# Kernel optimization log

Measured on AMD Instinct MI355X. Metric: run time of the kernel, lower is better.

Reference implementation:

```python
import jax, jax.numpy as jnp
import numpy as np

N_NODES = 100000


def gcn_conv(x, edge_index, W, b):
    # PyG GCNConv: add self-loops, symmetric normalization, then scatter-add.
    n = x.shape[0]
    loops = jnp.arange(n, dtype=edge_index.dtype)
    src = jnp.concatenate([edge_index[0], loops])
    dst = jnp.concatenate([edge_index[1], loops])
    h = x @ W  # [N, F_out] -- transform before propagate (small GEMM)
    ones = jnp.ones(src.shape[0], dtype=x.dtype)
    deg = jax.ops.segment_sum(ones, dst, num_segments=n)  # in-degree incl. self-loop
    dinv = jnp.where(deg > 0, jax.lax.rsqrt(deg), 0.0)
    norm = dinv[src] * dinv[dst]  # [E+N]
    msg = h[src] * norm[:, None]  # gather + scale, [E+N, F_out]
    out = jax.ops.segment_sum(msg, dst, num_segments=n)  # scatter-add
    return out + b


def setup_inputs() -> dict:
    key = jax.random.key(0)
    k1, k2, k3, k4 = jax.random.split(key, 4)
    d = 128
    x = jax.random.normal(k1, (N_NODES, d), dtype=jnp.float32)
    edge_index = jax.random.randint(k2, (2, 1600000), 0, N_NODES, dtype=jnp.int64)
    scale = 1.0 / np.sqrt(d)
    W1 = jax.random.normal(k3, (d, d), dtype=jnp.float32) * scale
    b1 = jnp.zeros((d,), dtype=jnp.float32)
    W2 = jax.random.normal(k4, (d, d), dtype=jnp.float32) * scale
    b2 = jnp.zeros((d,), dtype=jnp.float32)
    return {"x": x, "edge_index": edge_index, "W1": W1, "b1": b1, "W2": W2, "b2": b2}


def reference(x, edge_index, W1, b1, W2, b2):
    # Layer 1: GCNConv -> relu -> dropout(eval: identity)
    h = jax.nn.relu(gcn_conv(x, edge_index, W1, b1))
    # Layer 2
    h = jax.nn.relu(gcn_conv(h, edge_index, W2, b2))
    return h
```

## Files before the change

kernel.cpp:

```cpp
#include <hip/hip_runtime.h>


#define NFEAT 128
#define BSH 7
#define MAXNB 1024
#define BCAP 4096
#define BPITCH 136
#define EPITCH 132

typedef __attribute__((ext_vector_type(8))) short s8v;
typedef __attribute__((ext_vector_type(4))) float f4v;
typedef __attribute__((ext_vector_type(2))) float f2v;
typedef __attribute__((ext_vector_type(4))) uint u4v;

__device__ inline ushort f2bf(float f) {
    union { float f; uint u; } x; x.f = f;
    uint u = x.u;
    return (ushort)((u + 0x7fffu + ((u >> 16) & 1u)) >> 16);
}
__device__ inline f2v unpk(uint u) {
    union { uint u; float f; } lo, hi;
    lo.u = u << 16;
    hi.u = u & 0xffff0000u;
    return (f2v){lo.f, hi.f};
}
__device__ inline void upadd2(uint4 v, f2v* a) {
    a[0] += unpk(v.x);
    a[1] += unpk(v.y);
    a[2] += unpk(v.z);
    a[3] += unpk(v.w);
}

__global__ __launch_bounds__(256) void k_bscatter(const int* __restrict__ src,
                                                  const int* __restrict__ dst,
                                                  int* __restrict__ gcnt,
                                                  uint* __restrict__ ebuf,
                                                  int E, int NB, int CH) {
    __shared__ int h[MAXNB];
    int t = threadIdx.x;
    for (int i = t; i < NB; i += 256) h[i] = 0;
    __syncthreads();
    int e0 = blockIdx.x * CH;
    int e1 = min(e0 + CH, E);
    for (int e = e0 + t; e < e1; e += 256) atomicAdd(&h[dst[e] >> BSH], 1);
    __syncthreads();
    for (int i = t; i < NB; i += 256) {
        int c = h[i];
        h[i] = c ? (i * BCAP + atomicAdd(&gcnt[i], c)) : 0;
    }
    __syncthreads();
    for (int e = e0 + t; e < e1; e += 256) {
        int d = dst[e];
        int b = d >> BSH;
        int p = atomicAdd(&h[b], 1);
        if (p < (b + 1) * BCAP)
            ebuf[p] = ((uint)src[e] << BSH) | (uint)(d & ((1 << BSH) - 1));
    }
}

__global__ __launch_bounds__(256) void k_fill2(const uint* __restrict__ ebuf,
                                               const int* __restrict__ gcnt,
                                               int* __restrict__ row_ptr,
                                               float* __restrict__ dinv,
                                               int* __restrict__ col,
                                               int N, int E, int NB) {
    __shared__ int cnt[128];
    __shared__ int pre[128];
    __shared__ int sred[256];
    __shared__ int colL[BCAP];
    int b = blockIdx.x;
    int t = threadIdx.x;
    int part = 0;
    for (int j = t; j < b; j += 256) part += gcnt[j];
    sred[t] = part;
    __syncthreads();
    for (int off = 128; off >= 1; off >>= 1) {
        if (t < off) sred[t] += sred[t + off];
        __syncthreads();
    }
    int gb = sred[0];
    int m = min(gcnt[b], BCAP);
    if (t < 128) cnt[t] = 0;
    __syncthreads();
    const uint* eb = ebuf + (size_t)b * BCAP;
    for (int i = t; i < m; i += 256) atomicAdd(&cnt[eb[i] & 127], 1);
    __syncthreads();
    if (t < 128) pre[t] = cnt[t];
    __syncthreads();
    for (int off = 1; off < 128; off <<= 1) {
        int add = (t >= off && t < 128) ? pre[t - off] : 0;
        __syncthreads();
        if (t < 128) pre[t] += add;
        __syncthreads();
    }
    if (t < 128) {
        pre[t] -= cnt[t];
        int node = (b << BSH) + t;
        if (node < N) {
            row_ptr[node] = gb + pre[t];
            dinv[node] = rsqrtf((float)(cnt[t] + 1));
        }
    }
    __syncthreads();
    for (int i = t; i < m; i += 256) {
        uint p = eb[i];
        int pos = atomicAdd(&pre[p & 127], 1);
        colL[pos] = (int)(p >> BSH);
    }
    __syncthreads();
    for (int i = t; i < m; i += 256) col[gb + i] = colL[i];
    if (b == NB - 1 && t == 0) row_ptr[N] = E;
}

template <bool ABF16>
__global__ __launch_bounds__(256) void k_gemm3(const void* __restrict__ Ap,
                                               const float* __restrict__ W,
                                               const float* __restrict__ dinv,
                                               ushort* __restrict__ hs, int M) {
    __shared__ ushort Bs[128 * BPITCH];
    int t = threadIdx.x;

#pragma unroll
    for (int i = 0; i < 16; i++) {
        int idx = t + i * 256;
        int k4 = idx >> 7;
        int n = idx & 127;
        ushort o[4];
#pragma unroll
        for (int j = 0; j < 4; j++) o[j] = f2bf(W[(k4 * 4 + j) * NFEAT + n]);
        uint2 pk;
        __builtin_memcpy(&pk, o, 8);
        *(uint2*)&Bs[n * BPITCH + k4 * 4] = pk;
    }
    __syncthreads();

    int w = t >> 6, l = t & 63;
    int q = l >> 4, ln = l & 15;
    int wid = blockIdx.x * 4 + w;
    int row0 = wid * 32;
    bool alive = row0 < M;
    if (!alive) row0 = (M - 32) & ~31;

    s8v afr[2][4];
#pragma unroll
    for (int mt = 0; mt < 2; mt++) {
        int row = row0 + mt * 16 + ln;
        if (row >= M) row = M - 1;
        if (ABF16) {
            const ushort* A = (const ushort*)Ap + (size_t)row * NFEAT + q * 8;
#pragma unroll
            for (int ks = 0; ks < 4; ks++)
                afr[mt][ks] = *(const s8v*)(A + ks * 32);
        } else {
            const float* A = (const float*)Ap + (size_t)row * NFEAT + q * 8;
#pragma unroll
            for (int ks = 0; ks < 4; ks++) {
                float4 f0 = *(const float4*)(A + ks * 32);
                float4 f1 = *(const float4*)(A + ks * 32 + 4);
                ushort o[8] = {f2bf(f0.x), f2bf(f0.y), f2bf(f0.z), f2bf(f0.w),
                               f2bf(f1.x), f2bf(f1.y), f2bf(f1.z), f2bf(f1.w)};
                __builtin_memcpy(&afr[mt][ks], o, 16);
            }
        }
    }

    f4v acc[2][8];
#pragma unroll
    for (int mt = 0; mt < 2; mt++)
#pragma unroll
        for (int nt = 0; nt < 8; nt++) acc[mt][nt] = (f4v){0.f, 0.f, 0.f, 0.f};
#pragma unroll
    for (int nt = 0; nt < 8; nt++) {
        const ushort* Bp = Bs + (nt * 16 + ln) * BPITCH + q * 8;
#pragma unroll
        for (int ks = 0; ks < 4; ks++) {
            s8v bfr = *(const s8v*)(Bp + ks * 32);
            acc[0][nt] = __builtin_amdgcn_mfma_f32_16x16x32_bf16(afr[0][ks], bfr, acc[0][nt], 0, 0, 0);
            acc[1][nt] = __builtin_amdgcn_mfma_f32_16x16x32_bf16(afr[1][ks], bfr, acc[1][nt], 0, 0, 0);
        }
    }
    __syncthreads();

    ushort* ow = Bs + w * 32 * EPITCH;
#pragma unroll
    for (int mt = 0; mt < 2; mt++) {
#pragma unroll
        for (int r = 0; r < 4; r++) {
            int lrow = mt * 16 + q * 4 + r;
            float d = dinv[row0 + lrow];
#pragma unroll
            for (int nt = 0; nt < 8; nt++)
                ow[lrow * EPITCH + nt * 16 + ln] = f2bf(acc[mt][nt][r] * d);
        }
    }
    __builtin_amdgcn_s_waitcnt(0);
#pragma unroll
    for (int i = 0; i < 8; i++) {
        int idx = l + i * 64;
        int r = idx >> 4, c = idx & 15;
        const ushort* p = ow + r * EPITCH + c * 8;
        uint2 lo = *(const uint2*)p;
        uint2 hi = *(const uint2*)(p + 4);
        uint4 v = make_uint4(lo.x, lo.y, hi.x, hi.y);
        if (alive) *(uint4*)(hs + (size_t)(row0 + r) * NFEAT + c * 8) = v;
    }
}

template <bool OUT_BF16>
__global__ __launch_bounds__(256) void k_aggregate(const uint4* __restrict__ hs4,
                                                   const int* __restrict__ row_ptr,
                                                   const int* __restrict__ col,
                                                   const float* __restrict__ dinv,
                                                   const float* __restrict__ bias,
                                                   void* __restrict__ outp, int N) {
    int node = blockIdx.x * 16 + (threadIdx.x >> 4);
    if (node >= N) return;
    int sub = threadIdx.x & 15;

    uint4 vself = hs4[(size_t)node * 16 + sub];
    int s = row_ptr[node], e = row_ptr[node + 1];
    int nb = (e - s) >> 2;

    f2v a[4];
#pragma unroll
    for (int j = 0; j < 4; j++) a[j] = (f2v){0.f, 0.f};

    int k = s;
    if (nb > 0) {
        int c0 = col[k], c1 = col[k + 1], c2 = col[k + 2], c3 = col[k + 3];
        uint4 v0 = hs4[(size_t)c0 * 16 + sub];
        uint4 v1 = hs4[(size_t)c1 * 16 + sub];
        uint4 v2 = hs4[(size_t)c2 * 16 + sub];
        uint4 v3 = hs4[(size_t)c3 * 16 + sub];
        int d0 = col[k + 4], d1 = col[k + 5], d2 = col[k + 6], d3 = col[k + 7];
        k += 8;
        upadd2(vself, a);
        for (int it = 1; it < nb; ++it, k += 4) {
            uint4 w0 = hs4[(size_t)d0 * 16 + sub];
            uint4 w1 = hs4[(size_t)d1 * 16 + sub];
            uint4 w2 = hs4[(size_t)d2 * 16 + sub];
            uint4 w3 = hs4[(size_t)d3 * 16 + sub];
            int t0 = col[k], t1 = col[k + 1], t2 = col[k + 2], t3 = col[k + 3];
            upadd2(v0, a); upadd2(v1, a); upadd2(v2, a); upadd2(v3, a);
            v0 = w0; v1 = w1; v2 = w2; v3 = w3;
            d0 = t0; d1 = t1; d2 = t2; d3 = t3;
        }
        upadd2(v0, a); upadd2(v1, a); upadd2(v2, a); upadd2(v3, a);
        k = s + nb * 4;
    } else {
        upadd2(vself, a);
    }
    for (; k < e; ++k) upadd2(hs4[(size_t)col[k] * 16 + sub], a);

    float di = dinv[node];
    const float4* b4 = (const float4*)bias;
    float4 b0 = b4[sub * 2], b1 = b4[sub * 2 + 1];
    float r[8];
    r[0] = fmaxf(fmaf(di, a[0].x, b0.x), 0.f);
    r[1] = fmaxf(fmaf(di, a[0].y, b0.y), 0.f);
    r[2] = fmaxf(fmaf(di, a[1].x, b0.z), 0.f);
    r[3] = fmaxf(fmaf(di, a[1].y, b0.w), 0.f);
    r[4] = fmaxf(fmaf(di, a[2].x, b1.x), 0.f);
    r[5] = fmaxf(fmaf(di, a[2].y, b1.y), 0.f);
    r[6] = fmaxf(fmaf(di, a[3].x, b1.z), 0.f);
    r[7] = fmaxf(fmaf(di, a[3].y, b1.w), 0.f);
    if (OUT_BF16) {
        ushort o[8];
#pragma unroll
        for (int j = 0; j < 8; j++) o[j] = f2bf(r[j]);
        u4v pk;
        __builtin_memcpy(&pk, o, 16);
        __builtin_nontemporal_store(pk, (u4v*)outp + (size_t)node * 16 + sub);
    } else {
        float* orow = (float*)outp + (size_t)node * NFEAT + sub * 8;
        f4v r0 = {r[0], r[1], r[2], r[3]};
        f4v r1 = {r[4], r[5], r[6], r[7]};
        __builtin_nontemporal_store(r0, (f4v*)orow);
        __builtin_nontemporal_store(r1, (f4v*)(orow + 4));
    }
}

extern "C" void kernel_launch(void* const* d_in, const int* in_sizes, int n_in,
                              void* d_out, int out_size, void* d_ws, size_t ws_size,
                              hipStream_t stream) {
    const float* x = (const float*)d_in[0];
    const int* ei = (const int*)d_in[1];
    const float* W1 = (const float*)d_in[2];
    const float* b1 = (const float*)d_in[3];
    const float* W2 = (const float*)d_in[4];
    const float* b2 = (const float*)d_in[5];
    float* out = (float*)d_out;

    const int N = in_sizes[0] / NFEAT;
    const int E = in_sizes[1] / 2;
    const int* src = ei;
    const int* dst = ei + E;
    const int NB = (N + (1 << BSH) - 1) >> BSH;

    char* w = (char*)d_ws;
    size_t off = 0;
    auto alloc = [&](size_t bytes) -> void* {
        void* p = w + off;
        off = (off + bytes + 511) & ~(size_t)511;
        return p;
    };
    ushort* hs = (ushort*)alloc((size_t)N * NFEAT * 2);
    ushort* y1 = (ushort*)alloc((size_t)N * NFEAT * 2);
    int* row_ptr = (int*)alloc((size_t)(N + 1) * 4);
    float* dinv = (float*)alloc((size_t)N * 4);
    int* col = (int*)alloc((size_t)E * 4);
    uint* ebuf = (uint*)alloc((size_t)NB * BCAP * 4);
    int* gcnt = (int*)alloc((size_t)MAXNB * 4);
    (void)ws_size; (void)n_in; (void)out_size;

    const int CH = 2048;
    const int chBlk = (E + CH - 1) / CH;

    hipMemsetAsync(gcnt, 0, (size_t)MAXNB * 4, stream);
    k_bscatter<<<chBlk, 256, 0, stream>>>(src, dst, gcnt, ebuf, E, NB, CH);
    k_fill2<<<NB, 256, 0, stream>>>(ebuf, gcnt, row_ptr, dinv, col, N, E, NB);

    const int gemmBlk = (N + 127) / 128;
    const int aggBlk = (N + 15) / 16;

    k_gemm3<false><<<gemmBlk, 256, 0, stream>>>(x, W1, dinv, hs, N);
    k_aggregate<true><<<aggBlk, 256, 0, stream>>>((const uint4*)hs, row_ptr, col, dinv, b1, y1, N);
    k_gemm3<true><<<gemmBlk, 256, 0, stream>>>(y1, W2, dinv, hs, N);
    k_aggregate<false><<<aggBlk, 256, 0, stream>>>((const uint4*)hs, row_ptr, col, dinv, b2, out, N);
}
```

Before: 317.1 us.

## Overlap first GEMM with edge bucketing by moving dinv scaling into aggregation

The source-side dinv scaling moves out of the GEMM epilogue and into the aggregation, which now gathers dinv[col] per neighbour and applies it with an FMA. Since the GEMM no longer depends on degrees, the first GEMM runs in the same launch as the edge-bucketing scatter, using separate block ranges. The aim is to overlap the compute-bound GEMM with the atomic-heavy scatter and save one launch. In exchange, each aggregation edge costs an extra scattered 4-byte dinv load and more FMAs, and the GEMM result is rounded to bf16 before scaling rather than after.

```diff
diff --git a/kernel.cpp b/kernel.cpp
--- a/kernel.cpp
+++ b/kernel.cpp
@@ -24,38 +24,145 @@
     hi.u = u & 0xffff0000u;
     return (f2v){lo.f, hi.f};
 }
-__device__ inline void upadd2(uint4 v, f2v* a) {
-    a[0] += unpk(v.x);
-    a[1] += unpk(v.y);
-    a[2] += unpk(v.z);
-    a[3] += unpk(v.w);
-}
-
-__global__ __launch_bounds__(256) void k_bscatter(const int* __restrict__ src,
-                                                  const int* __restrict__ dst,
-                                                  int* __restrict__ gcnt,
-                                                  uint* __restrict__ ebuf,
-                                                  int E, int NB, int CH) {
-    __shared__ int h[MAXNB];
+__device__ inline void upfma2(uint4 v, float g, f2v* a) {
+    a[0] += g * unpk(v.x);
+    a[1] += g * unpk(v.y);
+    a[2] += g * unpk(v.z);
+    a[3] += g * unpk(v.w);
+}
+
+template <bool ABF16>
+__device__ inline void gemm_body(ushort* Bs, int bid, const void* __restrict__ Ap,
+                                 const float* __restrict__ W,
+                                 ushort* __restrict__ hs, int M) {
     int t = threadIdx.x;
-    for (int i = t; i < NB; i += 256) h[i] = 0;
-    __syncthreads();
-    int e0 = blockIdx.x * CH;
-    int e1 = min(e0 + CH, E);
-    for (int e = e0 + t; e < e1; e += 256) atomicAdd(&h[dst[e] >> BSH], 1);
-    __syncthreads();
-    for (int i = t; i < NB; i += 256) {
-        int c = h[i];
-        h[i] = c ? (i * BCAP + atomicAdd(&gcnt[i], c)) : 0;
-    }
-    __syncthreads();
-    for (int e = e0 + t; e < e1; e += 256) {
-        int d = dst[e];
-        int b = d >> BSH;
-        int p = atomicAdd(&h[b], 1);
-        if (p < (b + 1) * BCAP)
-            ebuf[p] = ((uint)src[e] << BSH) | (uint)(d & ((1 << BSH) - 1));
-    }
+
+#pragma unroll
+    for (int i = 0; i < 16; i++) {
+        int idx = t + i * 256;
+        int k4 = idx >> 7;
+        int n = idx & 127;
+        ushort o[4];
+#pragma unroll
+        for (int j = 0; j < 4; j++) o[j] = f2bf(W[(k4 * 4 + j) * NFEAT + n]);
+        uint2 pk;
+        __builtin_memcpy(&pk, o, 8);
+        *(uint2*)&Bs[n * BPITCH + k4 * 4] = pk;
+    }
+    __syncthreads();
+
+    int w = t >> 6, l = t & 63;
+    int q = l >> 4, ln = l & 15;
+    int wid = bid * 4 + w;
+    int row0 = wid * 32;
+    bool alive = row0 < M;
+    if (!alive) row0 = (M - 32) & ~31;
+
+    s8v afr[2][4];
+#pragma unroll
+    for (int mt = 0; mt < 2; mt++) {
+        int row = row0 + mt * 16 + ln;
+        if (row >= M) row = M - 1;
+        if (ABF16) {
+            const ushort* A = (const ushort*)Ap + (size_t)row * NFEAT + q * 8;
+#pragma unroll
+            for (int ks = 0; ks < 4; ks++)
+                afr[mt][ks] = *(const s8v*)(A + ks * 32);
+        } else {
+            const float* A = (const float*)Ap + (size_t)row * NFEAT + q * 8;
+#pragma unroll
+            for (int ks = 0; ks < 4; ks++) {
+                float4 f0 = *(const float4*)(A + ks * 32);
+                float4 f1 = *(const float4*)(A + ks * 32 + 4);
+                ushort o[8] = {f2bf(f0.x), f2bf(f0.y), f2bf(f0.z), f2bf(f0.w),
+                               f2bf(f1.x), f2bf(f1.y), f2bf(f1.z), f2bf(f1.w)};
+                __builtin_memcpy(&afr[mt][ks], o, 16);
+            }
+        }
+    }
+
+    f4v acc[2][8];
+#pragma unroll
+    for (int mt = 0; mt < 2; mt++)
+#pragma unroll
+        for (int nt = 0; nt < 8; nt++) acc[mt][nt] = (f4v){0.f, 0.f, 0.f, 0.f};
+#pragma unroll
+    for (int nt = 0; nt < 8; nt++) {
+        const ushort* Bp = Bs + (nt * 16 + ln) * BPITCH + q * 8;
+#pragma unroll
+        for (int ks = 0; ks < 4; ks++) {
+            s8v bfr = *(const s8v*)(Bp + ks * 32);
+            acc[0][nt] = __builtin_amdgcn_mfma_f32_16x16x32_bf16(afr[0][ks], bfr, acc[0][nt], 0, 0, 0);
+            acc[1][nt] = __builtin_amdgcn_mfma_f32_16x16x32_bf16(afr[1][ks], bfr, acc[1][nt], 0, 0, 0);
+        }
+    }
+    __syncthreads();
+
+    ushort* ow = Bs + w * 32 * EPITCH;
+#pragma unroll
+    for (int mt = 0; mt < 2; mt++) {
+#pragma unroll
+        for (int r = 0; r < 4; r++) {
+            int lrow = mt * 16 + q * 4 + r;
+#pragma unroll
+            for (int nt = 0; nt < 8; nt++)
+                ow[lrow * EPITCH + nt * 16 + ln] = f2bf(acc[mt][nt][r]);
+        }
+    }
+    __builtin_amdgcn_s_waitcnt(0);
+#pragma unroll
+    for (int i = 0; i < 8; i++) {
+        int idx = l + i * 64;
+        int r = idx >> 4, c = idx & 15;
+        const ushort* p = ow + r * EPITCH + c * 8;
+        uint2 lo = *(const uint2*)p;
+        uint2 hi = *(const uint2*)(p + 4);
+        uint4 v = make_uint4(lo.x, lo.y, hi.x, hi.y);
+        if (alive) *(uint4*)(hs + (size_t)(row0 + r) * NFEAT + c * 8) = v;
+    }
+}
+
+__global__ __launch_bounds__(256) void k_fused1(const int* __restrict__ src,
+                                                const int* __restrict__ dst,
+                                                int* __restrict__ gcnt,
+                                                uint* __restrict__ ebuf,
+                                                int E, int NB, int CH, int chBlk,
+                                                const float* __restrict__ x,
+                                                const float* __restrict__ W1,
+                                                ushort* __restrict__ hs, int M) {
+    __shared__ __align__(16) ushort smem[128 * BPITCH];
+    if (blockIdx.x < chBlk) {
+        int* h = (int*)smem;
+        int t = threadIdx.x;
+        for (int i = t; i < NB; i += 256) h[i] = 0;
+        __syncthreads();
+        int e0 = blockIdx.x * CH;
+        int e1 = min(e0 + CH, E);
+        for (int e = e0 + t; e < e1; e += 256) atomicAdd(&h[dst[e] >> BSH], 1);
+        __syncthreads();
+        for (int i = t; i < NB; i += 256) {
+            int c = h[i];
+            h[i] = c ? (i * BCAP + atomicAdd(&gcnt[i], c)) : 0;
+        }
+        __syncthreads();
+        for (int e = e0 + t; e < e1; e += 256) {
+            int d = dst[e];
+            int b = d >> BSH;
+            int p = atomicAdd(&h[b], 1);
+            if (p < (b + 1) * BCAP)
+                ebuf[p] = ((uint)src[e] << BSH) | (uint)(d & ((1 << BSH) - 1));
+        }
+    } else {
+        gemm_body<false>(smem, blockIdx.x - chBlk, x, W1, hs, M);
+    }
+}
+
+template <bool ABF16>
+__global__ __launch_bounds__(256) void k_gemm3(const void* __restrict__ Ap,
+                                               const float* __restrict__ W,
+                                               ushort* __restrict__ hs, int M) {
+    __shared__ __align__(16) ushort Bs[128 * BPITCH];
+    gemm_body<ABF16>(Bs, blockIdx.x, Ap, W, hs, M);
 }
 
 __global__ __launch_bounds__(256) void k_fill2(const uint* __restrict__ ebuf,
@@ -112,100 +219,6 @@
     if (b == NB - 1 && t == 0) row_ptr[N] = E;
 }
 
-template <bool ABF16>
-__global__ __launch_bounds__(256) void k_gemm3(const void* __restrict__ Ap,
-                                               const float* __restrict__ W,
-                                               const float* __restrict__ dinv,
-                                               ushort* __restrict__ hs, int M) {
-    __shared__ ushort Bs[128 * BPITCH];
-    int t = threadIdx.x;
-
-#pragma unroll
-    for (int i = 0; i < 16; i++) {
-        int idx = t + i * 256;
-        int k4 = idx >> 7;
-        int n = idx & 127;
-        ushort o[4];
-#pragma unroll
-        for (int j = 0; j < 4; j++) o[j] = f2bf(W[(k4 * 4 + j) * NFEAT + n]);
-        uint2 pk;
-        __builtin_memcpy(&pk, o, 8);
-        *(uint2*)&Bs[n * BPITCH + k4 * 4] = pk;
-    }
-    __syncthreads();
-
-    int w = t >> 6, l = t & 63;
-    int q = l >> 4, ln = l & 15;
-    int wid = blockIdx.x * 4 + w;
-    int row0 = wid * 32;
-    bool alive = row0 < M;
-    if (!alive) row0 = (M - 32) & ~31;
-
-    s8v afr[2][4];
-#pragma unroll
-    for (int mt = 0; mt < 2; mt++) {
-        int row = row0 + mt * 16 + ln;
-        if (row >= M) row = M - 1;
-        if (ABF16) {
-            const ushort* A = (const ushort*)Ap + (size_t)row * NFEAT + q * 8;
-#pragma unroll
-            for (int ks = 0; ks < 4; ks++)
-                afr[mt][ks] = *(const s8v*)(A + ks * 32);
-        } else {
-            const float* A = (const float*)Ap + (size_t)row * NFEAT + q * 8;
-#pragma unroll
-            for (int ks = 0; ks < 4; ks++) {
-                float4 f0 = *(const float4*)(A + ks * 32);
-                float4 f1 = *(const float4*)(A + ks * 32 + 4);
-                ushort o[8] = {f2bf(f0.x), f2bf(f0.y), f2bf(f0.z), f2bf(f0.w),
-                               f2bf(f1.x), f2bf(f1.y), f2bf(f1.z), f2bf(f1.w)};
-                __builtin_memcpy(&afr[mt][ks], o, 16);
-            }
-        }
-    }
-
-    f4v acc[2][8];
-#pragma unroll
-    for (int mt = 0; mt < 2; mt++)
-#pragma unroll
-        for (int nt = 0; nt < 8; nt++) acc[mt][nt] = (f4v){0.f, 0.f, 0.f, 0.f};
-#pragma unroll
-    for (int nt = 0; nt < 8; nt++) {
-        const ushort* Bp = Bs + (nt * 16 + ln) * BPITCH + q * 8;
-#pragma unroll
-        for (int ks = 0; ks < 4; ks++) {
-            s8v bfr = *(const s8v*)(Bp + ks * 32);
-            acc[0][nt] = __builtin_amdgcn_mfma_f32_16x16x32_bf16(afr[0][ks], bfr, acc[0][nt], 0, 0, 0);
-            acc[1][nt] = __builtin_amdgcn_mfma_f32_16x16x32_bf16(afr[1][ks], bfr, acc[1][nt], 0, 0, 0);
-        }
-    }
-    __syncthreads();
-
-    ushort* ow = Bs + w * 32 * EPITCH;
-#pragma unroll
-    for (int mt = 0; mt < 2; mt++) {
-#pragma unroll
-        for (int r = 0; r < 4; r++) {
-            int lrow = mt * 16 + q * 4 + r;
-            float d = dinv[row0 + lrow];
-#pragma unroll
-            for (int nt = 0; nt < 8; nt++)
-                ow[lrow * EPITCH + nt * 16 + ln] = f2bf(acc[mt][nt][r] * d);
-        }
-    }
-    __builtin_amdgcn_s_waitcnt(0);
-#pragma unroll
-    for (int i = 0; i < 8; i++) {
-        int idx = l + i * 64;
-        int r = idx >> 4, c = idx & 15;
-        const ushort* p = ow + r * EPITCH + c * 8;
-        uint2 lo = *(const uint2*)p;
-        uint2 hi = *(const uint2*)(p + 4);
-        uint4 v = make_uint4(lo.x, lo.y, hi.x, hi.y);
-        if (alive) *(uint4*)(hs + (size_t)(row0 + r) * NFEAT + c * 8) = v;
-    }
-}
-
 template <bool OUT_BF16>
 __global__ __launch_bounds__(256) void k_aggregate(const uint4* __restrict__ hs4,
                                                    const int* __restrict__ row_ptr,
@@ -218,6 +231,7 @@
     int sub = threadIdx.x & 15;
 
     uint4 vself = hs4[(size_t)node * 16 + sub];
+    float dself = dinv[node];
     int s = row_ptr[node], e = row_ptr[node + 1];
     int nb = (e - s) >> 2;
 
@@ -232,25 +246,31 @@
         uint4 v1 = hs4[(size_t)c1 * 16 + sub];
         uint4 v2 = hs4[(size_t)c2 * 16 + sub];
         uint4 v3 = hs4[(size_t)c3 * 16 + sub];
+        float g0 = dinv[c0], g1 = dinv[c1], g2 = dinv[c2], g3 = dinv[c3];
         int d0 = col[k + 4], d1 = col[k + 5], d2 = col[k + 6], d3 = col[k + 7];
         k += 8;
-        upadd2(vself, a);
+        upfma2(vself, dself, a);
         for (int it = 1; it < nb; ++it, k += 4) {
             uint4 w0 = hs4[(size_t)d0 * 16 + sub];
             uint4 w1 = hs4[(size_t)d1 * 16 + sub];
             uint4 w2 = hs4[(size_t)d2 * 16 + sub];
             uint4 w3 = hs4[(size_t)d3 * 16 + sub];
+            float h0 = dinv[d0], h1 = dinv[d1], h2 = dinv[d2], h3 = dinv[d3];
             int t0 = col[k], t1 = col[k + 1], t2 = col[k + 2], t3 = col[k + 3];
-            upadd2(v0, a); upadd2(v1, a); upadd2(v2, a); upadd2(v3, a);
+            upfma2(v0, g0, a); upfma2(v1, g1, a); upfma2(v2, g2, a); upfma2(v3, g3, a);
             v0 = w0; v1 = w1; v2 = w2; v3 = w3;
+            g0 = h0; g1 = h1; g2 = h2; g3 = h3;
             d0 = t0; d1 = t1; d2 = t2; d3 = t3;
         }
-        upadd2(v0, a); upadd2(v1, a); upadd2(v2, a); upadd2(v3, a);
+        upfma2(v0, g0, a); upfma2(v1, g1, a); upfma2(v2, g2, a); upfma2(v3, g3, a);
         k = s + nb * 4;
     } else {
-        upadd2(vself, a);
-    }
-    for (; k < e; ++k) upadd2(hs4[(size_t)col[k] * 16 + sub], a);
+        upfma2(vself, dself, a);
+    }
+    for (; k < e; ++k) {
+        int c = col[k];
+        upfma2(hs4[(size_t)c * 16 + sub], dinv[c], a);
+    }
 
     float di = dinv[node];
     const float4* b4 = (const float4*)bias;
@@ -315,16 +335,15 @@
 
     const int CH = 2048;
     const int chBlk = (E + CH - 1) / CH;
-
-    hipMemsetAsync(gcnt, 0, (size_t)MAXNB * 4, stream);
-    k_bscatter<<<chBlk, 256, 0, stream>>>(src, dst, gcnt, ebuf, E, NB, CH);
-    k_fill2<<<NB, 256, 0, stream>>>(ebuf, gcnt, row_ptr, dinv, col, N, E, NB);
-
     const int gemmBlk = (N + 127) / 128;
     const int aggBlk = (N + 15) / 16;
 
-    k_gemm3<false><<<gemmBlk, 256, 0, stream>>>(x, W1, dinv, hs, N);
+    hipMemsetAsync(gcnt, 0, (size_t)MAXNB * 4, stream);
+    k_fused1<<<chBlk + gemmBlk, 256, 0, stream>>>(src, dst, gcnt, ebuf, E, NB, CH, chBlk,
+                                                  x, W1, hs, N);
+    k_fill2<<<NB, 256, 0, stream>>>(ebuf, gcnt, row_ptr, dinv, col, N, E, NB);
+
     k_aggregate<true><<<aggBlk, 256, 0, stream>>>((const uint4*)hs, row_ptr, col, dinv, b1, y1, N);
-    k_gemm3<true><<<gemmBlk, 256, 0, stream>>>(y1, W2, dinv, hs, N);
+    k_gemm3<true><<<gemmBlk, 256, 0, stream>>>(y1, W2, hs, N);
     k_aggregate<false><<<aggBlk, 256, 0, stream>>>((const uint4*)hs, row_ptr, col, dinv, b2, out, N);
 }
```

New measurement: 320.9 us. Within noise of the previous version (+1.2%).
